# Optimization experiments

Measured on AMD Instinct MI355X. Metric: run time of the kernel, lower is better.

Reference implementation:

```python
import jax, jax.numpy as jnp
import numpy as np

NUM_HEADS = 8
IN_CH = 256  # C per branch; x has 2*C channels
DHW = (16, 16, 16)


def _proj(w, b, feat):
    # 1x1x1 Conv3d == per-voxel linear over channels. w: [Co, Ci], feat: [B, Ci, D, H, W]
    return jnp.einsum('oc,bcdhw->bodhw', w, feat) + b[None, :, None, None, None]


def _rope(n, dim):
    # matches rotary_embedding: returns [dim, n]
    inv_freq = 1.0 / (10000.0 ** (jnp.arange(0, dim, 2, dtype=jnp.float32) / dim))
    pos = jnp.linspace(-1.0, 1.0, n)
    sinusoid = pos[:, None] * inv_freq[None, :]          # [n, dim//2]
    emb = jnp.concatenate([jnp.sin(sinusoid), jnp.cos(sinusoid)], axis=-1)  # [n, dim]
    return emb.T                                          # [dim, n]


def setup_inputs() -> dict:
    key = jax.random.key(0)
    ks = jax.random.split(key, 5)
    D, H, W = DHW
    C = IN_CH
    s = 0.05
    return {
        'x': jax.random.normal(ks[0], (1, 2 * C, D, H, W), dtype=jnp.float32),
        'wq': jax.random.normal(ks[1], (C, C), dtype=jnp.float32) * s,
        'bq': jnp.zeros((C,), jnp.float32),
        'wk': jax.random.normal(ks[2], (C, C), dtype=jnp.float32) * s,
        'bk': jnp.zeros((C,), jnp.float32),
        'wv': jax.random.normal(ks[3], (C, C), dtype=jnp.float32) * s,
        'bv': jnp.zeros((C,), jnp.float32),
        'wo': jax.random.normal(ks[4], (2 * C, C), dtype=jnp.float32) * s,
        'bo': jnp.zeros((2 * C,), jnp.float32),
    }


def reference(x, wq, bq, wk, bk, wv, bv, wo, bo):
    qf, kvf = jnp.split(x, 2, axis=1)          # each [B, C, D, H, W]
    B, C, D, H, W = qf.shape
    hd = C // NUM_HEADS
    N = D * H * W
    q = _proj(wq, bq, qf).reshape(B, NUM_HEADS, hd, N)
    k = _proj(wk, bk, kvf).reshape(B, NUM_HEADS, hd, N)
    v = _proj(wv, bv, kvf).reshape(B, NUM_HEADS, hd, N)
    pe = _rope(N, hd)                           # [hd, N]
    q = q * pe[None, None]
    k = k * pe[None, None]
    attn = jnp.einsum('bhcn,bhcm->bhnm', q, k)  # note: no 1/sqrt(d) scaling, as in source
    attn = jax.nn.softmax(attn, axis=-1)
    out = jnp.einsum('bhnm,bhcm->bhcn', attn, v).reshape(B, C, D, H, W)
    return _proj(wo, bo, out + qf)              # [B, 2C, D, H, W]
```

## Files before the change

### kernel.cpp

```cpp
#include <hip/hip_runtime.h>
#include <hip/hip_bf16.h>

#define CIN 256
#define NV 4096
#define NHEAD 8
#define HD 32
#define NSPLIT 4
#define KSPAN (NV / NSPLIT)
#define LOG2E 1.44269504088896340736f
#define LOG2_10K_16 0.8304820237218405f

typedef __attribute__((ext_vector_type(8))) short short8;
typedef __attribute__((ext_vector_type(4))) float f32x4;

static __device__ __forceinline__ unsigned short f2bf(float f) {
    union { float f; unsigned u; } v; v.f = f;
    unsigned r = v.u + 0x7fffu + ((v.u >> 16) & 1u);
    return (unsigned short)(r >> 16);
}
static __device__ __forceinline__ unsigned pk_bf2(float x0, float x1) {
    return __builtin_amdgcn_perm(__float_as_uint(x1), __float_as_uint(x0),
                                 0x07060302u);
}
static __device__ __forceinline__ float bflo(unsigned u) {
    return __uint_as_float(u << 16);
}
static __device__ __forceinline__ float bfhi(unsigned u) {
    return __uint_as_float(u & 0xffff0000u);
}

__global__ __launch_bounds__(256) void conv_w(
    const float* __restrict__ wq, const float* __restrict__ wk,
    const float* __restrict__ wv, const float* __restrict__ wo,
    unsigned short* __restrict__ Wb)
{
    int i = (blockIdx.x * 256 + threadIdx.x) * 4;
    if (i >= 327680) return;
    const float* src;
    int off = i;
    if (i < 65536) { src = wq; }
    else if (i < 131072) { src = wk; off = i - 65536; }
    else if (i < 196608) { src = wv; off = i - 131072; }
    else { src = wo; off = i - 196608; }
    float4 v = *(const float4*)&src[off];
    unsigned short pk[4] = {f2bf(v.x), f2bf(v.y), f2bf(v.z), f2bf(v.w)};
    *(uint2*)&Wb[i] = *(uint2*)pk;
}

__global__ __launch_bounds__(512) void qkv_fused(
    const float* __restrict__ x, const unsigned short* __restrict__ Wb,
    const float* __restrict__ bq, const float* __restrict__ bk,
    const float* __restrict__ bv,
    unsigned short* __restrict__ Qbf, unsigned short* __restrict__ Kbf,
    unsigned short* __restrict__ Vbf)
{
    const int which = blockIdx.z;
    const unsigned short* Wp = Wb + (size_t)which * 65536;
    const float* Bp = (which == 0) ? bq : (which == 1) ? bk : bv;
    const int cbase = (which == 0) ? 0 : CIN;

    const int n0 = blockIdx.x * 32;
    const int m0 = blockIdx.y * 128;
    const int t = threadIdx.x;

    __shared__ __align__(16) unsigned short Sbuf[32 * 264];

    {
        const int n = t & 31, cg = t >> 5;
#pragma unroll 4
        for (int cc = 0; cc < 16; cc += 2) {
            const int c = cg * 16 + cc;
            size_t off = (size_t)(cbase + c) * NV + n0 + n;
            *(unsigned*)&Sbuf[n * 264 + c] = pk_bf2(x[off], x[off + NV]);
        }
    }
    __syncthreads();

    const int w = t >> 6;
    const int lane = t & 63;
    const int ln = lane & 15;
    const int quad = lane >> 4;
    const int M = m0 + w * 16 + ln;

    f32x4 acc[2] = {};
    const unsigned short* Wrow = &Wp[(size_t)M * 256 + quad * 8];
    for (int k0 = 0; k0 < 256; k0 += 32) {
        short8 a = *(const short8*)&Wrow[k0];
        short8 b[2];
#pragma unroll
        for (int nt = 0; nt < 2; ++nt)
            b[nt] = *(const short8*)&Sbuf[(nt * 16 + ln) * 264 + k0 + quad * 8];
        if (which == 2) {
#pragma unroll
            for (int nt = 0; nt < 2; ++nt)
                acc[nt] = __builtin_amdgcn_mfma_f32_16x16x32_bf16(
                    b[nt], a, acc[nt], 0, 0, 0);
        } else {
#pragma unroll
            for (int nt = 0; nt < 2; ++nt)
                acc[nt] = __builtin_amdgcn_mfma_f32_16x16x32_bf16(
                    a, b[nt], acc[nt], 0, 0, 0);
        }
    }
    __syncthreads();

    if (which == 2) {
        const int cl = w * 16 + ln;
        const float bias = Bp[m0 + cl];
#pragma unroll
        for (int nt = 0; nt < 2; ++nt) {
            unsigned short pk4[4];
#pragma unroll
            for (int r = 0; r < 4; ++r) pk4[r] = f2bf(acc[nt][r] + bias);
            *(uint2*)&Sbuf[cl * 40 + nt * 16 + quad * 4] = *(uint2*)pk4;
        }
        __syncthreads();
        {
            const int cl2 = t >> 2, q = t & 3;
            uint2 lo = *(const uint2*)&Sbuf[cl2 * 40 + q * 4];
            uint2 hi = *(const uint2*)&Sbuf[cl2 * 40 + 16 + q * 4];
            uint4 v;
            v.x = lo.x; v.y = lo.y; v.z = hi.x; v.w = hi.y;
            *(uint4*)&Vbf[(size_t)(m0 + cl2) * NV + n0 + q * 8] = v;
        }
    } else {
        const int mb = m0 + w * 16 + quad * 4;
        const int cb = mb & 31;
        const float qscale = (which == 0) ? LOG2E : 1.0f;
        float bias[4], invf[4];
#pragma unroll
        for (int r = 0; r < 4; ++r) {
            bias[r] = Bp[mb + r];
            invf[r] = __builtin_amdgcn_exp2f(
                -(float)((cb + r) & 15) * LOG2_10K_16);
        }
        const bool use_sin = (cb < 16);
        const int ml = w * 16 + quad * 4;
#pragma unroll
        for (int nt = 0; nt < 2; ++nt) {
            const int n = n0 + nt * 16 + ln;
            const float pos = (float)n * (2.0f / 4095.0f) - 1.0f;
#pragma unroll
            for (int r = 0; r < 4; ++r) {
                float ang = pos * invf[r];
                float f = (use_sin ? __sinf(ang) : __cosf(ang)) * qscale;
                Sbuf[(nt * 16 + ln) * 264 + ml + r] =
                    f2bf((acc[nt][r] + bias[r]) * f);
            }
        }
        __syncthreads();
        unsigned short* dst = (which == 0) ? Qbf : Kbf;
        const int h0 = m0 >> 5;
        {
            const int hh = t >> 7;
            const int n = (t >> 2) & 31;
            const int cw = t & 3;
            uint4 v = *(const uint4*)&Sbuf[n * 264 + hh * 32 + cw * 8];
            *(uint4*)&dst[((size_t)(h0 + hh) * NV + n0 + n) * HD + cw * 8] = v;
        }
    }
}

__global__ __launch_bounds__(256, 4) void attn_mfma(
    const unsigned short* __restrict__ Qbf,
    const unsigned short* __restrict__ Kbf,
    const unsigned short* __restrict__ Vbf,
    unsigned short* __restrict__ Opartb, float* __restrict__ Lpart)
{
    const int l = blockIdx.x + (blockIdx.y << 6) + (blockIdx.z << 9);
    const int pr = l & 31;
    const int h = pr & 7;
    const int z = pr >> 3;
    const int q0 = (l >> 5) * 64;
    const int kbase = z * KSPAN;
    const int t = threadIdx.x;
    const int w = t >> 6;
    const int lane = t & 63;
    const int ln = lane & 15;
    const int quad = lane >> 4;

    __shared__ __align__(16) char Smem[33792];
    unsigned short* Ks = (unsigned short*)Smem;
    unsigned short* Vs = (unsigned short*)(Smem + 16384);

    short8 qa[4];
#pragma unroll
    for (int qt = 0; qt < 4; ++qt)
        qa[qt] = *(const short8*)
            &Qbf[((size_t)h * NV + q0 + qt * 16 + ln) * HD + quad * 8];

    const unsigned short* Kh = Kbf + (size_t)h * NV * HD;
    const unsigned short* Vh = Vbf + (size_t)h * HD * NV;

    const int cv = t >> 3;
    const unsigned short* gsrcV = Vh + (size_t)cv * NV + ((t & 7) ^ (cv & 7)) * 8;
    const int kv = t >> 2;
    const unsigned short* gsrcK =
        Kh + (size_t)kv * HD + ((t & 3) ^ (kv & 3)) * 8;

    f32x4 oacc[4][2] = {};
    f32x4 lacc[4] = {};
    const short vone = (short)0x3F80;
    const short8 vones = {vone, vone, vone, vone, vone, vone, vone, vone};

    __builtin_amdgcn_global_load_lds(
        (const __attribute__((address_space(1))) unsigned int*)(gsrcK +
            (size_t)kbase * HD),
        (__attribute__((address_space(3))) unsigned int*)&Ks[t * 8], 16, 0, 0);
    __builtin_amdgcn_global_load_lds(
        (const __attribute__((address_space(1))) unsigned int*)(gsrcK +
            (size_t)(kbase + 64) * HD),
        (__attribute__((address_space(3))) unsigned int*)&Ks[2048 + t * 8],
        16, 0, 0);
    __builtin_amdgcn_global_load_lds(
        (const __attribute__((address_space(1))) unsigned int*)(gsrcV + kbase),
        (__attribute__((address_space(3))) unsigned int*)&Vs[t * 8], 16, 0, 0);
    __builtin_amdgcn_global_load_lds(
        (const __attribute__((address_space(1))) unsigned int*)(gsrcV + kbase +
            64),
        (__attribute__((address_space(3))) unsigned int*)&Vs[2048 + t * 8],
        16, 0, 0);
    __syncthreads();

    const int sgk = (quad ^ (ln & 3)) * 8;
    const int wsub = (w >> 1) * 2048;
    const int wh = w & 1;

    for (int i = 0; i < KSPAN / 128; ++i) {
        const int kb = kbase + i * 128;
        const int buf = (i & 1) * 4096;

        if (i + 1 < KSPAN / 128) {
            const int nb = buf ^ 4096;
            __builtin_amdgcn_global_load_lds(
                (const __attribute__((address_space(1))) unsigned int*)(gsrcK +
                    (size_t)(kb + 128) * HD),
                (__attribute__((address_space(3))) unsigned int*)&Ks[nb + t * 8],
                16, 0, 0);
            __builtin_amdgcn_global_load_lds(
                (const __attribute__((address_space(1))) unsigned int*)(gsrcK +
                    (size_t)(kb + 192) * HD),
                (__attribute__((address_space(3))) unsigned int*)&Ks[nb + 2048 +
                    t * 8],
                16, 0, 0);
            __builtin_amdgcn_global_load_lds(
                (const __attribute__((address_space(1))) unsigned int*)(gsrcV +
                    kb + 128),
                (__attribute__((address_space(3))) unsigned int*)&Vs[nb + t * 8],
                16, 0, 0);
            __builtin_amdgcn_global_load_lds(
                (const __attribute__((address_space(1))) unsigned int*)(gsrcV +
                    kb + 192),
                (__attribute__((address_space(3))) unsigned int*)&Vs[nb + 2048 +
                    t * 8],
                16, 0, 0);
        }

        const unsigned short* Kb = &Ks[buf + wsub];
        const unsigned short* Vb = &Vs[buf + wsub];
        const short8 kf0 = *(const short8*)&Kb[(wh * 32 + ln) * 32 + sgk];
        const short8 kf1 = *(const short8*)&Kb[(wh * 32 + 16 + ln) * 32 + sgk];
        const int cA0 = ln, cA1 = 16 + ln;
        const short8 vb0 = *(const short8*)
            &Vb[cA0 * 64 + (((wh * 4 + quad) ^ (cA0 & 7)) * 8)];
        const short8 vb1 = *(const short8*)
            &Vb[cA1 * 64 + (((wh * 4 + quad) ^ (cA1 & 7)) * 8)];

#pragma unroll
        for (int qt = 0; qt < 4; ++qt) {
            f32x4 z4 = {0.f, 0.f, 0.f, 0.f};
            __builtin_amdgcn_s_setprio(1);
            f32x4 s0 = __builtin_amdgcn_mfma_f32_16x16x32_bf16(kf0, qa[qt],
                                                               z4, 0, 0, 0);
            f32x4 s1 = __builtin_amdgcn_mfma_f32_16x16x32_bf16(kf1, qa[qt],
                                                               z4, 0, 0, 0);
            __builtin_amdgcn_s_setprio(0);

            float p0[4], p1[4];
#pragma unroll
            for (int r = 0; r < 4; ++r) {
                p0[r] = __builtin_amdgcn_exp2f(s0[r]);
                p1[r] = __builtin_amdgcn_exp2f(s1[r]);
            }
            short8 pa;
            unsigned* pau = (unsigned*)&pa;
            pau[0] = pk_bf2(p0[0], p0[1]);
            pau[1] = pk_bf2(p0[2], p0[3]);
            pau[2] = pk_bf2(p1[0], p1[1]);
            pau[3] = pk_bf2(p1[2], p1[3]);

            __builtin_amdgcn_s_setprio(1);
            lacc[qt] = __builtin_amdgcn_mfma_f32_16x16x32_bf16(pa, vones,
                                                               lacc[qt],
                                                               0, 0, 0);
            oacc[qt][0] = __builtin_amdgcn_mfma_f32_16x16x32_bf16(
                pa, vb0, oacc[qt][0], 0, 0, 0);
            oacc[qt][1] = __builtin_amdgcn_mfma_f32_16x16x32_bf16(
                pa, vb1, oacc[qt][1], 0, 0, 0);
            __builtin_amdgcn_s_setprio(0);
        }
        __syncthreads();
    }

    float* Ored = (float*)Smem;
    float* lred = (float*)(Smem + 32768);
#pragma unroll
    for (int qt = 0; qt < 4; ++qt) {
#pragma unroll
        for (int ct = 0; ct < 2; ++ct)
            *(f32x4*)&Ored[(((w * 4 + qt) * 2 + ct) << 8) + lane * 4] =
                oacc[qt][ct];
        if (ln == 0)
            *(f32x4*)&lred[(w * 4 + qt) * 16 + quad * 4] = lacc[qt];
    }
    __syncthreads();

    f32x4 of0 = {}, of1 = {}, lf = {};
#pragma unroll
    for (int w2 = 0; w2 < 4; ++w2) {
        of0 += *(const f32x4*)&Ored[(((w2 * 4 + w) * 2 + 0) << 8) + lane * 4];
        of1 += *(const f32x4*)&Ored[(((w2 * 4 + w) * 2 + 1) << 8) + lane * 4];
        lf  += *(const f32x4*)&lred[(w2 * 4 + w) * 16 + quad * 4];
    }

    unsigned short* Oz = Opartb + (size_t)z * CIN * NV;
    float* Lz = Lpart + (size_t)z * NHEAD * NV;
    if (ln == 0) {
#pragma unroll
        for (int r = 0; r < 4; ++r)
            Lz[(size_t)h * NV + q0 + w * 16 + quad * 4 + r] = lf[r];
    }
    {
        uint2 st;
        st.x = pk_bf2(of0[0], of0[1]);
        st.y = pk_bf2(of0[2], of0[3]);
        *(uint2*)&Oz[(size_t)(h * HD + ln) * NV + q0 + w * 16 + quad * 4] = st;
        st.x = pk_bf2(of1[0], of1[1]);
        st.y = pk_bf2(of1[2], of1[3]);
        *(uint2*)&Oz[(size_t)(h * HD + 16 + ln) * NV + q0 + w * 16 +
                     quad * 4] = st;
    }
}

__global__ __launch_bounds__(512) void out_fused(
    const float* __restrict__ x,
    const unsigned short* __restrict__ Opartb,
    const float* __restrict__ Lpart,
    const unsigned short* __restrict__ Wob, const float* __restrict__ bo,
    float* __restrict__ out)
{
    const int n0 = blockIdx.x * 32;
    const int m0 = blockIdx.y * 128;
    const int t = threadIdx.x;

    __shared__ __align__(16) unsigned short Ys[32 * 264];

    {
        const int n2 = (t & 15) * 2;
        const int grp = t >> 4;
        const int h = grp >> 2;
        const size_t lo = (size_t)h * NV + n0 + n2;
        float l0 = 0.f, l1 = 0.f;
#pragma unroll
        for (int zz = 0; zz < NSPLIT; ++zz) {
            l0 += Lpart[(size_t)zz * NHEAD * NV + lo];
            l1 += Lpart[(size_t)zz * NHEAD * NV + lo + 1];
        }
        const float rl0 = __builtin_amdgcn_rcpf(l0);
        const float rl1 = __builtin_amdgcn_rcpf(l1);
#pragma unroll
        for (int i = 0; i < 8; ++i) {
            const int c = grp * 8 + i;
            size_t off = (size_t)c * NV + n0 + n2;
            float s0 = 0.f, s1 = 0.f;
#pragma unroll
            for (int zz = 0; zz < NSPLIT; ++zz) {
                unsigned o = *(const unsigned*)&Opartb[(size_t)zz * CIN * NV + off];
                s0 += bflo(o);
                s1 += bfhi(o);
            }
            float2 x2 = *(const float2*)&x[off];
            Ys[n2 * 264 + c] = f2bf(s0 * rl0 + x2.x);
            Ys[(n2 + 1) * 264 + c] = f2bf(s1 * rl1 + x2.y);
        }
    }
    __syncthreads();

    const int w = t >> 6;
    const int lane = t & 63;
    const int ln = lane & 15;
    const int quad = lane >> 4;
    const int M = m0 + w * 16 + ln;

    const unsigned short* Wrow = &Wob[(size_t)M * 256 + quad * 8];
    f32x4 acc[2] = {};
    for (int k0 = 0; k0 < 256; k0 += 32) {
        short8 a = *(const short8*)&Wrow[k0];
        short8 b[2];
#pragma unroll
        for (int nt = 0; nt < 2; ++nt)
            b[nt] = *(const short8*)&Ys[(nt * 16 + ln) * 264 + k0 + quad * 8];
#pragma unroll
        for (int nt = 0; nt < 2; ++nt)
            acc[nt] = __builtin_amdgcn_mfma_f32_16x16x32_bf16(
                a, b[nt], acc[nt], 0, 0, 0);
    }

    const int mb = m0 + w * 16 + quad * 4;
    float bias[4];
#pragma unroll
    for (int r = 0; r < 4; ++r) bias[r] = bo[mb + r];
#pragma unroll
    for (int nt = 0; nt < 2; ++nt)
#pragma unroll
        for (int r = 0; r < 4; ++r)
            out[(size_t)(mb + r) * NV + n0 + nt * 16 + ln] =
                acc[nt][r] + bias[r];
}

extern "C" void kernel_launch(void* const* d_in, const int* in_sizes, int n_in,
                              void* d_out, int out_size, void* d_ws,
                              size_t ws_size, hipStream_t stream)
{
    const float* x  = (const float*)d_in[0];
    const float* wq = (const float*)d_in[1];
    const float* bq = (const float*)d_in[2];
    const float* wk = (const float*)d_in[3];
    const float* bk = (const float*)d_in[4];
    const float* wv = (const float*)d_in[5];
    const float* bv = (const float*)d_in[6];
    const float* wo = (const float*)d_in[7];
    const float* bo = (const float*)d_in[8];
    float* out = (float*)d_out;

    unsigned short* Wb  = (unsigned short*)d_ws;
    unsigned short* Qbf = Wb + 327680;
    unsigned short* Kbf = Qbf + (size_t)CIN * NV;
    unsigned short* Vbf = Kbf + (size_t)CIN * NV;
    float* Lpart = (float*)(Vbf + (size_t)CIN * NV);
    unsigned short* Opartb =
        (unsigned short*)(Lpart + NSPLIT * (size_t)NHEAD * NV);

    conv_w<<<dim3(320), 256, 0, stream>>>(wq, wk, wv, wo, Wb);
    qkv_fused<<<dim3(128, 2, 3), 512, 0, stream>>>(
        x, Wb, bq, bk, bv, Qbf, Kbf, Vbf);
    attn_mfma<<<dim3(NV / 64, NHEAD, NSPLIT), 256, 0, stream>>>(
        Qbf, Kbf, Vbf, Opartb, Lpart);
    out_fused<<<dim3(128, 4), 512, 0, stream>>>(
        x, Opartb, Lpart, Wb + 196608, bo, out);
}
```

Measured before the change: 121.7 us.

## Remove split-K in attention and normalize output inside attention kernel

Drops the four-way key split in the attention kernel so each block processes all keys for its query tile. The softmax normalization now happens in the attention epilogue, and a single bf16 output is written. This removes the partial-output and partial-sum buffers and the combine pass in the output projection kernel. The cost is a quarter as many attention blocks, which lowers occupancy on the GPU and makes each block's sequential loop longer.

```diff
diff --git a/kernel.cpp b/kernel.cpp
--- a/kernel.cpp
+++ b/kernel.cpp
@@ -5,8 +5,6 @@
 #define NV 4096
 #define NHEAD 8
 #define HD 32
-#define NSPLIT 4
-#define KSPAN (NV / NSPLIT)
 #define LOG2E 1.44269504088896340736f
 #define LOG2_10K_16 0.8304820237218405f
 
@@ -165,14 +163,11 @@
     const unsigned short* __restrict__ Qbf,
     const unsigned short* __restrict__ Kbf,
     const unsigned short* __restrict__ Vbf,
-    unsigned short* __restrict__ Opartb, float* __restrict__ Lpart)
+    unsigned short* __restrict__ Ybf)
 {
-    const int l = blockIdx.x + (blockIdx.y << 6) + (blockIdx.z << 9);
-    const int pr = l & 31;
-    const int h = pr & 7;
-    const int z = pr >> 3;
-    const int q0 = (l >> 5) * 64;
-    const int kbase = z * KSPAN;
+    const int l = blockIdx.x + (blockIdx.y << 6);
+    const int h = l & 7;
+    const int q0 = (l >> 3) * 64;
     const int t = threadIdx.x;
     const int w = t >> 6;
     const int lane = t & 63;
@@ -204,20 +199,18 @@
     const short8 vones = {vone, vone, vone, vone, vone, vone, vone, vone};
 
     __builtin_amdgcn_global_load_lds(
-        (const __attribute__((address_space(1))) unsigned int*)(gsrcK +
-            (size_t)kbase * HD),
+        (const __attribute__((address_space(1))) unsigned int*)gsrcK,
         (__attribute__((address_space(3))) unsigned int*)&Ks[t * 8], 16, 0, 0);
     __builtin_amdgcn_global_load_lds(
         (const __attribute__((address_space(1))) unsigned int*)(gsrcK +
-            (size_t)(kbase + 64) * HD),
+            (size_t)64 * HD),
         (__attribute__((address_space(3))) unsigned int*)&Ks[2048 + t * 8],
         16, 0, 0);
     __builtin_amdgcn_global_load_lds(
-        (const __attribute__((address_space(1))) unsigned int*)(gsrcV + kbase),
+        (const __attribute__((address_space(1))) unsigned int*)gsrcV,
         (__attribute__((address_space(3))) unsigned int*)&Vs[t * 8], 16, 0, 0);
     __builtin_amdgcn_global_load_lds(
-        (const __attribute__((address_space(1))) unsigned int*)(gsrcV + kbase +
-            64),
+        (const __attribute__((address_space(1))) unsigned int*)(gsrcV + 64),
         (__attribute__((address_space(3))) unsigned int*)&Vs[2048 + t * 8],
         16, 0, 0);
     __syncthreads();
@@ -226,11 +219,11 @@
     const int wsub = (w >> 1) * 2048;
     const int wh = w & 1;
 
-    for (int i = 0; i < KSPAN / 128; ++i) {
-        const int kb = kbase + i * 128;
+    for (int i = 0; i < NV / 128; ++i) {
+        const int kb = i * 128;
         const int buf = (i & 1) * 4096;
 
-        if (i + 1 < KSPAN / 128) {
+        if (i + 1 < NV / 128) {
             const int nb = buf ^ 4096;
             __builtin_amdgcn_global_load_lds(
                 (const __attribute__((address_space(1))) unsigned int*)(gsrcK +
@@ -323,29 +316,24 @@
         lf  += *(const f32x4*)&lred[(w2 * 4 + w) * 16 + quad * 4];
     }
 
-    unsigned short* Oz = Opartb + (size_t)z * CIN * NV;
-    float* Lz = Lpart + (size_t)z * NHEAD * NV;
-    if (ln == 0) {
-#pragma unroll
-        for (int r = 0; r < 4; ++r)
-            Lz[(size_t)h * NV + q0 + w * 16 + quad * 4 + r] = lf[r];
-    }
+    float rl[4];
+#pragma unroll
+    for (int r = 0; r < 4; ++r) rl[r] = __builtin_amdgcn_rcpf(lf[r]);
     {
         uint2 st;
-        st.x = pk_bf2(of0[0], of0[1]);
-        st.y = pk_bf2(of0[2], of0[3]);
-        *(uint2*)&Oz[(size_t)(h * HD + ln) * NV + q0 + w * 16 + quad * 4] = st;
-        st.x = pk_bf2(of1[0], of1[1]);
-        st.y = pk_bf2(of1[2], of1[3]);
-        *(uint2*)&Oz[(size_t)(h * HD + 16 + ln) * NV + q0 + w * 16 +
-                     quad * 4] = st;
+        st.x = pk_bf2(of0[0] * rl[0], of0[1] * rl[1]);
+        st.y = pk_bf2(of0[2] * rl[2], of0[3] * rl[3]);
+        *(uint2*)&Ybf[(size_t)(h * HD + ln) * NV + q0 + w * 16 + quad * 4] = st;
+        st.x = pk_bf2(of1[0] * rl[0], of1[1] * rl[1]);
+        st.y = pk_bf2(of1[2] * rl[2], of1[3] * rl[3]);
+        *(uint2*)&Ybf[(size_t)(h * HD + 16 + ln) * NV + q0 + w * 16 +
+                      quad * 4] = st;
     }
 }
 
 __global__ __launch_bounds__(512) void out_fused(
     const float* __restrict__ x,
-    const unsigned short* __restrict__ Opartb,
-    const float* __restrict__ Lpart,
+    const unsigned short* __restrict__ Ybf,
     const unsigned short* __restrict__ Wob, const float* __restrict__ bo,
     float* __restrict__ out)
 {
@@ -358,30 +346,14 @@
     {
         const int n2 = (t & 15) * 2;
         const int grp = t >> 4;
-        const int h = grp >> 2;
-        const size_t lo = (size_t)h * NV + n0 + n2;
-        float l0 = 0.f, l1 = 0.f;
-#pragma unroll
-        for (int zz = 0; zz < NSPLIT; ++zz) {
-            l0 += Lpart[(size_t)zz * NHEAD * NV + lo];
-            l1 += Lpart[(size_t)zz * NHEAD * NV + lo + 1];
-        }
-        const float rl0 = __builtin_amdgcn_rcpf(l0);
-        const float rl1 = __builtin_amdgcn_rcpf(l1);
 #pragma unroll
         for (int i = 0; i < 8; ++i) {
             const int c = grp * 8 + i;
             size_t off = (size_t)c * NV + n0 + n2;
-            float s0 = 0.f, s1 = 0.f;
-#pragma unroll
-            for (int zz = 0; zz < NSPLIT; ++zz) {
-                unsigned o = *(const unsigned*)&Opartb[(size_t)zz * CIN * NV + off];
-                s0 += bflo(o);
-                s1 += bfhi(o);
-            }
+            unsigned o = *(const unsigned*)&Ybf[off];
             float2 x2 = *(const float2*)&x[off];
-            Ys[n2 * 264 + c] = f2bf(s0 * rl0 + x2.x);
-            Ys[(n2 + 1) * 264 + c] = f2bf(s1 * rl1 + x2.y);
+            Ys[n2 * 264 + c] = f2bf(bflo(o) + x2.x);
+            Ys[(n2 + 1) * 264 + c] = f2bf(bfhi(o) + x2.y);
         }
     }
     __syncthreads();
@@ -437,15 +409,13 @@
     unsigned short* Qbf = Wb + 327680;
     unsigned short* Kbf = Qbf + (size_t)CIN * NV;
     unsigned short* Vbf = Kbf + (size_t)CIN * NV;
-    float* Lpart = (float*)(Vbf + (size_t)CIN * NV);
-    unsigned short* Opartb =
-        (unsigned short*)(Lpart + NSPLIT * (size_t)NHEAD * NV);
+    unsigned short* Ybf = Vbf + (size_t)CIN * NV;
 
     conv_w<<<dim3(320), 256, 0, stream>>>(wq, wk, wv, wo, Wb);
     qkv_fused<<<dim3(128, 2, 3), 512, 0, stream>>>(
         x, Wb, bq, bk, bv, Qbf, Kbf, Vbf);
-    attn_mfma<<<dim3(NV / 64, NHEAD, NSPLIT), 256, 0, stream>>>(
-        Qbf, Kbf, Vbf, Opartb, Lpart);
+    attn_mfma<<<dim3(NV / 64, NHEAD), 256, 0, stream>>>(
+        Qbf, Kbf, Vbf, Ybf);
     out_fused<<<dim3(128, 4), 512, 0, stream>>>(
-        x, Opartb, Lpart, Wb + 196608, bo, out);
-}
+        x, Ybf, Wb + 196608, bo, out);
+}
```

After: 120.1 us. No clear change (-1.4%).
